# Kernel tuning notes

Measured on AMD Instinct MI355X. Metric: run time of the kernel, lower is better.

Reference implementation:

```python
import jax, jax.numpy as jnp
import numpy as np

M = 16
C = 7 * M          # 112, stage-8 channels
CLS = 20
TOPK = 3
NQ = 20000         # current-frame active sites at stage 8
NS = 8192          # support-frame active sites at stage 8
SCALE = 128.0      # voxel coordinate range at this depth


def setup_inputs() -> dict:
    key = jax.random.key(0)
    ks = jax.random.split(key, 9)
    coords_q = jax.random.uniform(ks[0], (NQ, 3), jnp.float32) * SCALE
    coords_s = jax.random.uniform(ks[1], (NS, 3), jnp.float32) * SCALE
    x7 = jax.random.normal(ks[2], (NQ, C), jnp.float32)
    feat_s7 = jax.random.normal(ks[3], (NS, C), jnp.float32)
    feat_s = jax.random.normal(ks[4], (NS, C), jnp.float32)
    w_attn = jax.random.normal(ks[5], (C,), jnp.float32) * 0.1
    W1 = jax.random.normal(ks[6], (2 * C, C), jnp.float32) * (1.0 / np.sqrt(2 * C))
    gamma = jnp.ones((C,), jnp.float32)
    beta = jnp.zeros((C,), jnp.float32)
    W2 = jax.random.normal(ks[7], (C, C), jnp.float32) * (1.0 / np.sqrt(C))
    W_cls = jax.random.normal(ks[8], (C, CLS), jnp.float32) * (1.0 / np.sqrt(C))
    b_cls = jnp.zeros((CLS,), jnp.float32)
    return dict(coords_q=coords_q, coords_s=coords_s, x7=x7, feat_s7=feat_s7,
                feat_s=feat_s, w_attn=w_attn, W1=W1, gamma=gamma, beta=beta,
                W2=W2, W_cls=W_cls, b_cls=b_cls)


def reference(coords_q, coords_s, x7, feat_s7, feat_s, w_attn, W1, gamma, beta, W2, W_cls, b_cls):
    # GlobalMeanAttentionPooling: attention-weighted mean over support sites -> global vector [C]
    a = jax.nn.softmax(feat_s7 @ w_attn)          # [NS]
    g = a @ feat_s7                                # [C]
    # GlobalMaskLayer: channel-wise sigmoid gating of current-frame features
    feat_q = x7 * jax.nn.sigmoid(g)                # [NQ, C]
    # DistMatchLayer_v4: top-3 nearest support voxels per query, softmax(-d2) weighting
    q2 = jnp.sum(coords_q * coords_q, -1, keepdims=True)   # [NQ, 1]
    s2 = jnp.sum(coords_s * coords_s, -1)                  # [NS]
    d2 = q2 + s2[None, :] - 2.0 * (coords_q @ coords_s.T)  # [NQ, NS]
    negd, idx = jax.lax.top_k(-d2, TOPK)                   # [NQ, K]
    w = jax.nn.softmax(negd, axis=-1)                      # [NQ, K]
    matched = jnp.einsum('nk,nkc->nc', w, feat_s[idx])     # [NQ, C]
    # tune_sub: 1x1 subconv (14m->7m) -> BN(eval affine) + ReLU -> 1x1 subconv (7m->7m)
    h = jnp.concatenate([feat_q, matched], -1) @ W1        # [NQ, C]
    h = jax.nn.relu(h * gamma + beta) @ W2                 # [NQ, C]
    # final classifier linear
    return h @ W_cls + b_cls                               # [NQ, CLS]
```

## Files before the change

kernel.cpp:

```cpp
#include <hip/hip_runtime.h>

#define NQv 20000
#define NSv 8192
#define Cv  112
#define CLSv 20
#define INFF 3.4e38f
#define JINF 0x7fffffff

#define GC 16
#define NCELL 4096
#define CELLH 8.0f
#define INVH 0.125f

#define POOLB 32
#define PT 1024
#define PNW (POOLB * PT / 64)

#define MB (NQv / 32)
#define MT 512
#define WS_START 3616
#define WS_PTS4  5668
#define WS_W1TH  38440
#define WS_W1TL  50984
#define WS_W2TH  63528
#define WS_W2TL  70696
#define WS_WCT   77864

typedef __attribute__((ext_vector_type(8))) short bf16x8;
typedef __attribute__((ext_vector_type(4))) float f32x4;
typedef unsigned short us;
typedef unsigned long long u64;

__device__ __forceinline__ float bf2f(us u) {
    union { unsigned int i; float f; } v; v.i = ((unsigned int)u) << 16; return v.f;
}
__device__ __forceinline__ us f2bf(float f) {
    union { float f; unsigned int i; } v; v.f = f;
    unsigned int r = v.i + 0x7fffu + ((v.i >> 16) & 1u);
    return (us)(r >> 16);
}
__device__ __forceinline__ void split(float v, us& h, us& l) {
    h = f2bf(v); l = f2bf(v - bf2f(h));
}

__device__ __forceinline__ u64 mkkey(float e, int j) {
    union { float f; unsigned int i; } v; v.f = e;
    unsigned int ue = v.i ^ ((unsigned int)((int)v.i >> 31) | 0x80000000u);
    return ((u64)ue << 32) | (unsigned int)j;
}
__device__ __forceinline__ float keyval(u64 k) {
    unsigned int ue = (unsigned int)(k >> 32);
    unsigned int u = ue ^ ((unsigned int)((int)(~ue) >> 31) | 0x80000000u);
    union { unsigned int i; float f; } v; v.i = u; return v.f;
}
__device__ __forceinline__ u64 umin64(u64 a, u64 b) { return a < b ? a : b; }
__device__ __forceinline__ u64 umax64(u64 a, u64 b) { return a > b ? a : b; }

__global__ __launch_bounds__(PT) void k_prep(const float* __restrict__ cs,
                                             const float* __restrict__ fs7,
                                             const float* __restrict__ wat,
                                             const float* __restrict__ W1,
                                             const float* __restrict__ W2,
                                             const float* __restrict__ Wc,
                                             float* __restrict__ ws) {
    int b = blockIdx.x, tid = threadIdx.x;

    if (b == POOLB + 1) {
        us* w1h = (us*)(ws + WS_W1TH);
        us* w1l = (us*)(ws + WS_W1TL);
        for (int idx = tid; idx < Cv * 224; idx += PT) {
            int c = idx / 224, k = idx - c * 224;
            us h, l; split(W1[k * Cv + c], h, l);
            w1h[c * 224 + k] = h; w1l[c * 224 + k] = l;
        }
        return;
    }
    if (b == POOLB + 2) {
        us* w2h = (us*)(ws + WS_W2TH);
        us* w2l = (us*)(ws + WS_W2TL);
        for (int idx = tid; idx < Cv * 128; idx += PT) {
            int c = idx >> 7, k = idx & 127;
            float v = (k < Cv) ? W2[k * Cv + c] : 0.f;
            us h, l; split(v, h, l);
            w2h[c * 128 + k] = h; w2l[c * 128 + k] = l;
        }
        float* wct = ws + WS_WCT;
        for (int idx = tid; idx < CLSv * Cv; idx += PT) {
            int cls = idx / Cv, k = idx - cls * Cv;
            wct[cls * Cv + k] = Wc[k * CLSv + cls];
        }
        return;
    }
    if (b == POOLB) {
        __shared__ int cnt[NCELL];
        __shared__ int wsum[PT / 64];
        us* startg = (us*)(ws + WS_START);
        float4* pts4 = (float4*)(ws + WS_PTS4);
        int lane = tid & 63, wv = tid >> 6;
        for (int i = tid; i < NCELL; i += PT) cnt[i] = 0;
        __syncthreads();
        float xx[8], yy[8], zz[8]; int cid[8]; int pp[8];
        #pragma unroll
        for (int k = 0; k < NSv / PT; ++k) {
            int p = k * PT + tid;
            pp[k] = p;
            xx[k] = cs[3 * p]; yy[k] = cs[3 * p + 1]; zz[k] = cs[3 * p + 2];
            int cx = (int)(xx[k] * INVH), cy = (int)(yy[k] * INVH), cz = (int)(zz[k] * INVH);
            cx = cx > 15 ? 15 : cx; cy = cy > 15 ? 15 : cy; cz = cz > 15 ? 15 : cz;
            cid[k] = (cz * GC + cy) * GC + cx;
            atomicAdd(&cnt[cid[k]], 1);
        }
        __syncthreads();
        int base = tid * 4;
        int c0 = cnt[base], c1 = cnt[base + 1], c2 = cnt[base + 2], c3 = cnt[base + 3];
        int local = c0 + c1 + c2 + c3;
        int inc = local;
        #pragma unroll
        for (int off = 1; off < 64; off <<= 1) {
            int v = __shfl_up(inc, off, 64);
            if (lane >= off) inc += v;
        }
        if (lane == 63) wsum[wv] = inc;
        __syncthreads();
        if (tid < PT / 64) {
            int v = wsum[tid];
            #pragma unroll
            for (int off = 1; off < 16; off <<= 1) {
                int o = __shfl_up(v, off, 64);
                if (tid >= off) v += o;
            }
            wsum[tid] = v;
        }
        __syncthreads();
        int wbase = (wv == 0) ? 0 : wsum[wv - 1];
        int run = wbase + inc - local;
        startg[base] = (us)run;     cnt[base] = run;     run += c0;
        startg[base + 1] = (us)run; cnt[base + 1] = run; run += c1;
        startg[base + 2] = (us)run; cnt[base + 2] = run; run += c2;
        startg[base + 3] = (us)run; cnt[base + 3] = run;
        if (tid == 0) startg[NCELL] = (us)NSv;
        __syncthreads();
        #pragma unroll
        for (int k = 0; k < NSv / PT; ++k) {
            int slot = atomicAdd(&cnt[cid[k]], 1);
            pts4[slot] = make_float4(-2.f * xx[k], -2.f * yy[k], -2.f * zz[k], (float)pp[k]);
        }
        return;
    }

    __shared__ float red[PT / 64][Cv + 1];
    int gtid = b * PT + tid;
    int wid = gtid >> 6, lw = tid >> 6, lane = gtid & 63, l2 = lane * 2;
    float2 wa = make_float2(0.f, 0.f);
    if (lane < 56) wa = *(const float2*)(wat + l2);
    float gx = 0.f, gy = 0.f, z = 0.f;
    for (int g = 0; g < 2; ++g) {
        float2 f[8]; float part[8];
        #pragma unroll
        for (int u = 0; u < 8; ++u) {
            int i = wid + (g * 8 + u) * PNW;
            f[u] = (lane < 56) ? *(const float2*)(fs7 + i * Cv + l2) : make_float2(0.f, 0.f);
            part[u] = f[u].x * wa.x + f[u].y * wa.y;
        }
        #pragma unroll
        for (int off = 32; off; off >>= 1)
            #pragma unroll
            for (int u = 0; u < 8; ++u) part[u] += __shfl_xor(part[u], off, 64);
        #pragma unroll
        for (int u = 0; u < 8; ++u) {
            float p = __expf(part[u]);
            gx = fmaf(p, f[u].x, gx); gy = fmaf(p, f[u].y, gy); z += p;
        }
    }
    if (lane < 56) { red[lw][l2] = gx; red[lw][l2 + 1] = gy; }
    if (lane == 0) red[lw][Cv] = z;
    __syncthreads();
    if (tid < Cv + 1) {
        float s = 0.f;
        #pragma unroll
        for (int i = 0; i < PT / 64; ++i) s += red[i][tid];
        ws[b * (Cv + 1) + tid] = s;
    }
}

__device__ __forceinline__ void scan_run(const float4* __restrict__ pts4,
                                         int a, int b, float qx, float qy, float qz,
                                         float& E0, float& E1, float& E2,
                                         int& J0, int& J1, int& J2) {
    for (int k = a; k < b; ++k) {
        float4 P = pts4[k];
        float x = -0.5f * P.x, y = -0.5f * P.y, z = -0.5f * P.z;
        float s2 = fmaf(x, x, fmaf(y, y, z * z));
        float e = fmaf(qx, P.x, fmaf(qy, P.y, fmaf(qz, P.z, s2)));
        int j = (int)P.w;
        bool lt2 = (e < E2) || (e == E2 && j < J2);
        if (lt2) {
            bool lt1 = (e < E1) || (e == E1 && j < J1);
            bool lt0 = (e < E0) || (e == E0 && j < J0);
            E2 = lt1 ? E1 : e;              J2 = lt1 ? J1 : j;
            E1 = lt0 ? E0 : (lt1 ? e : E1); J1 = lt0 ? J0 : (lt1 ? j : J1);
            if (lt0) { E0 = e; J0 = j; }
        }
    }
}

__global__ __launch_bounds__(MT, 6) void k_fused(
        const float* __restrict__ cq,
        const float* __restrict__ x7, const float* __restrict__ fs,
        const float* __restrict__ gma, const float* __restrict__ bta,
        const float* __restrict__ bc, const float* __restrict__ ws,
        float* __restrict__ out) {
    __shared__ __align__(16) us vb[2 * 32 * 232];
    __shared__ __align__(16) us hbh[32 * 136];
    __shared__ __align__(16) us hbl[32 * 136];
    __shared__ float gate[Cv];
    __shared__ int   qi[32][3];
    __shared__ float qw[32][3];

    us* vbh = vb;
    us* vbl = vb + 32 * 232;
    float* h2f = (float*)vb;

    const us* __restrict__ startg = (const us*)(ws + WS_START);
    const float4* __restrict__ pts4 = (const float4*)(ws + WS_PTS4);

    int tid = threadIdx.x;
    int q0 = blockIdx.x * 32;

    int vq = tid / 14, ve = tid - vq * 14;
    float4 px[4];
    bool hasx = (tid < 448) && (ve < 7);
    if (hasx) {
        const float4* xr = (const float4*)(x7 + (q0 + vq) * Cv + ve * 16);
        px[0] = xr[0]; px[1] = xr[1]; px[2] = xr[2]; px[3] = xr[3];
    }

    if (tid < Cv) {
        float st = 0.f, zt = 0.f;
        for (int b = 0; b < POOLB; ++b) {
            st += ws[b * (Cv + 1) + tid];
            zt += ws[b * (Cv + 1) + Cv];
        }
        gate[tid] = 1.0f / (1.0f + __expf(-(st / zt)));
    }
    {
        int q = tid >> 4, kk = Cv + (tid & 15);
        hbh[q * 136 + kk] = 0; hbl[q * 136 + kk] = 0;
    }

    {
        int sub = tid & 15;
        int qq  = tid >> 4;
        int q   = q0 + qq;
        float qx = cq[3 * q], qy = cq[3 * q + 1], qz = cq[3 * q + 2];
        float q2 = fmaf(qx, qx, fmaf(qy, qy, qz * qz));
        int cx = (int)(qx * INVH), cy = (int)(qy * INVH), cz = (int)(qz * INVH);
        cx = cx > 15 ? 15 : cx; cy = cy > 15 ? 15 : cy; cz = cz > 15 ? 15 : cz;
        float E0 = INFF, E1 = INFF, E2 = INFF;
        int   J0 = JINF, J1 = JINF, J2 = JINF;

        #pragma unroll
        for (int c = sub; c < 27; c += 16) {
            int dz = c / 9 - 1, dy = (c / 3) % 3 - 1, dx = c % 3 - 1;
            int xc = cx + dx, yc = cy + dy, zc = cz + dz;
            if ((unsigned)xc < 16u && (unsigned)yc < 16u && (unsigned)zc < 16u) {
                int ccell = (zc * GC + yc) * GC + xc;
                scan_run(pts4, startg[ccell], startg[ccell + 1], qx, qy, qz,
                         E0, E1, E2, J0, J1, J2);
            }
        }

        u64 K0 = ~0ull, K1 = ~0ull, K2 = ~0ull;
        bool done = false;
        for (int s = 2; ; ++s) {
            if (!done) {
                K0 = mkkey(E0, J0); K1 = mkkey(E1, J1); K2 = mkkey(E2, J2);
                #pragma unroll
                for (int off = 1; off < 16; off <<= 1) {
                    u64 b0 = __shfl_xor(K0, off, 64);
                    u64 b1 = __shfl_xor(K1, off, 64);
                    u64 b2 = __shfl_xor(K2, off, 64);
                    u64 xx = umax64(K0, b0), yy = umin64(K1, b1);
                    u64 zz = umax64(K1, b1), uu = umin64(K2, b2);
                    K0 = umin64(K0, b0);
                    u64 n1 = umin64(xx, yy);
                    K2 = umin64(umin64(umax64(xx, yy), zz), uu);
                    K1 = n1;
                }
            }
            if (s > 15) break;
            if (!done) {
                int r = s - 1;
                int xl = cx - r > 0 ? cx - r : 0, xh = cx + r < 15 ? cx + r : 15;
                int yl = cy - r > 0 ? cy - r : 0, yh = cy + r < 15 ? cy + r : 15;
                int zl = cz - r > 0 ? cz - r : 0, zh = cz + r < 15 ? cz + r : 15;
                float fx = INFF, fy = INFF, fz = INFF;
                if (xl > 0)  fx = qx - xl * CELLH;
                if (xh < 15) fx = fminf(fx, (xh + 1) * CELLH - qx);
                if (yl > 0)  fy = qy - yl * CELLH;
                if (yh < 15) fy = fminf(fy, (yh + 1) * CELLH - qy);
                if (zl > 0)  fz = qz - zl * CELLH;
                if (zh < 15) fz = fminf(fz, (zh + 1) * CELLH - qz);
                float dmin = fminf(fx, fminf(fy, fz));
                float t2 = keyval(K2);
                if (dmin * dmin > t2 + q2 + 0.5f) {
                    done = true;
                } else {
                    int side = 2 * s + 1, s2n = side * side, tot = s2n * side;
                    for (int idx = sub; idx < tot; idx += 16) {
                        int dz = idx / s2n - s;
                        int rem = idx - (dz + s) * s2n;
                        int dy = rem / side - s;
                        int dx = rem - (dy + s) * side - s;
                        int ax = dx < 0 ? -dx : dx, ay = dy < 0 ? -dy : dy, az = dz < 0 ? -dz : dz;
                        if (ax != s && ay != s && az != s) continue;
                        int xc = cx + dx, yc = cy + dy, zc = cz + dz;
                        if ((unsigned)xc > 15u || (unsigned)yc > 15u || (unsigned)zc > 15u) continue;
                        int ccell = (zc * GC + yc) * GC + xc;
                        scan_run(pts4, startg[ccell], startg[ccell + 1], qx, qy, qz,
                                 E0, E1, E2, J0, J1, J2);
                    }
                }
            }
            if (__all(done)) break;
        }

        if (sub == 0) {
            unsigned int A0 = (unsigned int)K0;
            unsigned int A1 = (unsigned int)K1;
            unsigned int A2 = (unsigned int)K2;
            if (A0 >= NSv) A0 = 0;
            if (A1 >= NSv) A1 = 0;
            if (A2 >= NSv) A2 = 0;
            float e0 = keyval(K0), e1 = keyval(K1), e2 = keyval(K2);
            float w1v = __expf(e0 - e1);
            float w2v = __expf(e0 - e2);
            float iw  = 1.0f / (1.0f + w1v + w2v);
            qw[qq][0] = iw; qw[qq][1] = w1v * iw; qw[qq][2] = w2v * iw;
            qi[qq][0] = (int)A0; qi[qq][1] = (int)A1; qi[qq][2] = (int)A2;
        }
    }
    __syncthreads();

    if (tid < 448) {
        int k0 = ve * 16;
        float vals[16];
        if (ve < 7) {
            #pragma unroll
            for (int i = 0; i < 4; ++i) {
                float4 v = px[i];
                vals[i * 4]     = v.x * gate[k0 + i * 4];
                vals[i * 4 + 1] = v.y * gate[k0 + i * 4 + 1];
                vals[i * 4 + 2] = v.z * gate[k0 + i * 4 + 2];
                vals[i * 4 + 3] = v.w * gate[k0 + i * 4 + 3];
            }
        } else {
            int kk = k0 - Cv;
            float w0 = qw[vq][0], w1v = qw[vq][1], w2v = qw[vq][2];
            const float4* r0 = (const float4*)(fs + qi[vq][0] * Cv + kk);
            const float4* r1 = (const float4*)(fs + qi[vq][1] * Cv + kk);
            const float4* r2 = (const float4*)(fs + qi[vq][2] * Cv + kk);
            #pragma unroll
            for (int i = 0; i < 4; ++i) {
                float4 a = r0[i], b = r1[i], c = r2[i];
                vals[i * 4]     = w0 * a.x + w1v * b.x + w2v * c.x;
                vals[i * 4 + 1] = w0 * a.y + w1v * b.y + w2v * c.y;
                vals[i * 4 + 2] = w0 * a.z + w1v * b.z + w2v * c.z;
                vals[i * 4 + 3] = w0 * a.w + w1v * b.w + w2v * c.w;
            }
        }
        #pragma unroll
        for (int i = 0; i < 16; ++i) {
            us h, l; split(vals[i], h, l);
            vbh[vq * 232 + k0 + i] = h;
            vbl[vq * 232 + k0 + i] = l;
        }
    }
    __syncthreads();

    int w = tid >> 6, lane = tid & 63, quad = lane >> 4, l16 = lane & 15;
    int cc = w * 16 + l16;

    if (w < 7) {
        f32x4 acc0 = {0.f, 0.f, 0.f, 0.f};
        f32x4 acc1 = {0.f, 0.f, 0.f, 0.f};
        const us* w1h = (const us*)(ws + WS_W1TH) + cc * 224;
        const us* w1l = (const us*)(ws + WS_W1TL) + cc * 224;
        #pragma unroll
        for (int ks = 0; ks < 7; ++ks) {
            int ko = ks * 32 + quad * 8;
            bf16x8 bh  = *(const bf16x8*)(w1h + ko);
            bf16x8 bl  = *(const bf16x8*)(w1l + ko);
            bf16x8 a0h = *(const bf16x8*)(vbh + l16 * 232 + ko);
            bf16x8 a0l = *(const bf16x8*)(vbl + l16 * 232 + ko);
            bf16x8 a1h = *(const bf16x8*)(vbh + (l16 + 16) * 232 + ko);
            bf16x8 a1l = *(const bf16x8*)(vbl + (l16 + 16) * 232 + ko);
            acc0 = __builtin_amdgcn_mfma_f32_16x16x32_bf16(a0h, bh, acc0, 0, 0, 0);
            acc0 = __builtin_amdgcn_mfma_f32_16x16x32_bf16(a0l, bh, acc0, 0, 0, 0);
            acc0 = __builtin_amdgcn_mfma_f32_16x16x32_bf16(a0h, bl, acc0, 0, 0, 0);
            acc1 = __builtin_amdgcn_mfma_f32_16x16x32_bf16(a1h, bh, acc1, 0, 0, 0);
            acc1 = __builtin_amdgcn_mfma_f32_16x16x32_bf16(a1l, bh, acc1, 0, 0, 0);
            acc1 = __builtin_amdgcn_mfma_f32_16x16x32_bf16(a1h, bl, acc1, 0, 0, 0);
        }
        float g = gma[cc], bb = bta[cc];
        #pragma unroll
        for (int r = 0; r < 4; ++r) {
            int q = quad * 4 + r;
            float h = fmaf(acc0[r], g, bb); h = h > 0.f ? h : 0.f;
            us hh, ll; split(h, hh, ll);
            hbh[q * 136 + cc] = hh; hbl[q * 136 + cc] = ll;
            float h2 = fmaf(acc1[r], g, bb); h2 = h2 > 0.f ? h2 : 0.f;
            split(h2, hh, ll);
            hbh[(q + 16) * 136 + cc] = hh; hbl[(q + 16) * 136 + cc] = ll;
        }
    }
    __syncthreads();

    if (w < 7) {
        f32x4 acc0 = {0.f, 0.f, 0.f, 0.f};
        f32x4 acc1 = {0.f, 0.f, 0.f, 0.f};
        const us* w2h = (const us*)(ws + WS_W2TH) + cc * 128;
        const us* w2l = (const us*)(ws + WS_W2TL) + cc * 128;
        #pragma unroll
        for (int ks = 0; ks < 4; ++ks) {
            int ko = ks * 32 + quad * 8;
            bf16x8 bh  = *(const bf16x8*)(w2h + ko);
            bf16x8 bl  = *(const bf16x8*)(w2l + ko);
            bf16x8 a0h = *(const bf16x8*)(hbh + l16 * 136 + ko);
            bf16x8 a0l = *(const bf16x8*)(hbl + l16 * 136 + ko);
            bf16x8 a1h = *(const bf16x8*)(hbh + (l16 + 16) * 136 + ko);
            bf16x8 a1l = *(const bf16x8*)(hbl + (l16 + 16) * 136 + ko);
            acc0 = __builtin_amdgcn_mfma_f32_16x16x32_bf16(a0h, bh, acc0, 0, 0, 0);
            acc0 = __builtin_amdgcn_mfma_f32_16x16x32_bf16(a0l, bh, acc0, 0, 0, 0);
            acc0 = __builtin_amdgcn_mfma_f32_16x16x32_bf16(a0h, bl, acc0, 0, 0, 0);
            acc1 = __builtin_amdgcn_mfma_f32_16x16x32_bf16(a1h, bh, acc1, 0, 0, 0);
            acc1 = __builtin_amdgcn_mfma_f32_16x16x32_bf16(a1l, bh, acc1, 0, 0, 0);
            acc1 = __builtin_amdgcn_mfma_f32_16x16x32_bf16(a1h, bl, acc1, 0, 0, 0);
        }
        #pragma unroll
        for (int r = 0; r < 4; ++r) {
            int q = quad * 4 + r;
            h2f[q * 116 + cc] = acc0[r];
            h2f[(q + 16) * 116 + cc] = acc1[r];
        }
    }
    __syncthreads();

    for (int it = tid; it < 32 * CLSv; it += MT) {
        int cls = it % CLSv, qq = it / CLSv;
        const float4* wr = (const float4*)(ws + WS_WCT + cls * Cv);
        const float4* hr = (const float4*)(h2f + qq * 116);
        float a = bc[cls];
        #pragma unroll 7
        for (int i = 0; i < 28; ++i) {
            float4 h = hr[i], v = wr[i];
            a = fmaf(h.x, v.x, fmaf(h.y, v.y, fmaf(h.z, v.z, fmaf(h.w, v.w, a))));
        }
        out[(q0 + qq) * CLSv + cls] = a;
    }
}

extern "C" void kernel_launch(void* const* d_in, const int* in_sizes, int n_in,
                              void* d_out, int out_size, void* d_ws, size_t ws_size,
                              hipStream_t stream) {
    const float* cq  = (const float*)d_in[0];
    const float* cs  = (const float*)d_in[1];
    const float* x7  = (const float*)d_in[2];
    const float* fs7 = (const float*)d_in[3];
    const float* fs  = (const float*)d_in[4];
    const float* wat = (const float*)d_in[5];
    const float* W1  = (const float*)d_in[6];
    const float* gma = (const float*)d_in[7];
    const float* bta = (const float*)d_in[8];
    const float* W2  = (const float*)d_in[9];
    const float* Wc  = (const float*)d_in[10];
    const float* bc  = (const float*)d_in[11];
    float* ws  = (float*)d_ws;
    float* out = (float*)d_out;

    k_prep<<<POOLB + 3, PT, 0, stream>>>(cs, fs7, wat, W1, W2, Wc, ws);
    k_fused<<<MB, MT, 0, stream>>>(cq, x7, fs, gma, bta, bc, ws, out);
}
```

Measured before the change: 142.5 us.

## Halve queries per block to 16 and remap MFMA waves to column pairs

The fused kernel now handles 16 queries per block with 256 threads, which doubles the block count. In the two MFMA GEMMs each of the 4 waves now covers one 16-row tile and one or two 16-column output tiles, instead of 7 waves each covering two row tiles. The pooling partials are stored channel-major so the gate reduction reads contiguous memory, and the s==2 shell of the kNN search gets a specialized loop with constant divisors. The intent is better load balance and occupancy for the irregular kNN search, at the cost of reloading weight fragments per 16 queries and some wave imbalance (waves 0-2 do double work).

```diff
diff --git a/kernel.cpp b/kernel.cpp
--- a/kernel.cpp
+++ b/kernel.cpp
@@ -16,8 +16,9 @@
 #define PT 1024
 #define PNW (POOLB * PT / 64)
 
-#define MB (NQv / 32)
-#define MT 512
+#define MQ 16
+#define MB (NQv / MQ)
+#define MT 256
 #define WS_START 3616
 #define WS_PTS4  5668
 #define WS_W1TH  38440
@@ -179,7 +180,7 @@
         float s = 0.f;
         #pragma unroll
         for (int i = 0; i < PT / 64; ++i) s += red[i][tid];
-        ws[b * (Cv + 1) + tid] = s;
+        ws[tid * POOLB + b] = s;
     }
 }
 
@@ -210,26 +211,26 @@
         const float* __restrict__ gma, const float* __restrict__ bta,
         const float* __restrict__ bc, const float* __restrict__ ws,
         float* __restrict__ out) {
-    __shared__ __align__(16) us vb[2 * 32 * 232];
-    __shared__ __align__(16) us hbh[32 * 136];
-    __shared__ __align__(16) us hbl[32 * 136];
+    __shared__ __align__(16) us vb[2 * MQ * 232];
+    __shared__ __align__(16) us hbh[MQ * 136];
+    __shared__ __align__(16) us hbl[MQ * 136];
     __shared__ float gate[Cv];
-    __shared__ int   qi[32][3];
-    __shared__ float qw[32][3];
+    __shared__ int   qi[MQ][3];
+    __shared__ float qw[MQ][3];
 
     us* vbh = vb;
-    us* vbl = vb + 32 * 232;
+    us* vbl = vb + MQ * 232;
     float* h2f = (float*)vb;
 
     const us* __restrict__ startg = (const us*)(ws + WS_START);
     const float4* __restrict__ pts4 = (const float4*)(ws + WS_PTS4);
 
     int tid = threadIdx.x;
-    int q0 = blockIdx.x * 32;
+    int q0 = blockIdx.x * MQ;
 
     int vq = tid / 14, ve = tid - vq * 14;
     float4 px[4];
-    bool hasx = (tid < 448) && (ve < 7);
+    bool hasx = (tid < 224) && (ve < 7);
     if (hasx) {
         const float4* xr = (const float4*)(x7 + (q0 + vq) * Cv + ve * 16);
         px[0] = xr[0]; px[1] = xr[1]; px[2] = xr[2]; px[3] = xr[3];
@@ -237,10 +238,10 @@
 
     if (tid < Cv) {
         float st = 0.f, zt = 0.f;
-        for (int b = 0; b < POOLB; ++b) {
-            st += ws[b * (Cv + 1) + tid];
-            zt += ws[b * (Cv + 1) + Cv];
-        }
+        const float* pr = ws + tid * POOLB;
+        const float* zr = ws + Cv * POOLB;
+        #pragma unroll
+        for (int b = 0; b < POOLB; ++b) { st += pr[b]; zt += zr[b]; }
         gate[tid] = 1.0f / (1.0f + __expf(-(st / zt)));
     }
     {
@@ -305,6 +306,20 @@
                 float t2 = keyval(K2);
                 if (dmin * dmin > t2 + q2 + 0.5f) {
                     done = true;
+                } else if (s == 2) {
+                    for (int idx = sub; idx < 125; idx += 16) {
+                        int dz = idx / 25 - 2;
+                        int rem = idx - (dz + 2) * 25;
+                        int dy = rem / 5 - 2;
+                        int dx = rem - (dy + 2) * 5 - 2;
+                        int ax = dx < 0 ? -dx : dx, ay = dy < 0 ? -dy : dy, az = dz < 0 ? -dz : dz;
+                        if (ax != 2 && ay != 2 && az != 2) continue;
+                        int xc = cx + dx, yc = cy + dy, zc = cz + dz;
+                        if ((unsigned)xc > 15u || (unsigned)yc > 15u || (unsigned)zc > 15u) continue;
+                        int ccell = (zc * GC + yc) * GC + xc;
+                        scan_run(pts4, startg[ccell], startg[ccell + 1], qx, qy, qz,
+                                 E0, E1, E2, J0, J1, J2);
+                    }
                 } else {
                     int side = 2 * s + 1, s2n = side * side, tot = s2n * side;
                     for (int idx = sub; idx < tot; idx += 16) {
@@ -342,7 +357,7 @@
     }
     __syncthreads();
 
-    if (tid < 448) {
+    if (tid < 224) {
         int k0 = ve * 16;
         float vals[16];
         if (ve < 7) {
@@ -379,74 +394,87 @@
     __syncthreads();
 
     int w = tid >> 6, lane = tid & 63, quad = lane >> 4, l16 = lane & 15;
-    int cc = w * 16 + l16;
-
-    if (w < 7) {
+    bool two = (w < 3);
+    int cc0 = w * 16 + l16;
+    int cc1 = two ? (w + 4) * 16 + l16 : cc0;
+
+    {
         f32x4 acc0 = {0.f, 0.f, 0.f, 0.f};
         f32x4 acc1 = {0.f, 0.f, 0.f, 0.f};
-        const us* w1h = (const us*)(ws + WS_W1TH) + cc * 224;
-        const us* w1l = (const us*)(ws + WS_W1TL) + cc * 224;
+        const us* w1h0 = (const us*)(ws + WS_W1TH) + cc0 * 224;
+        const us* w1l0 = (const us*)(ws + WS_W1TL) + cc0 * 224;
+        const us* w1h1 = (const us*)(ws + WS_W1TH) + cc1 * 224;
+        const us* w1l1 = (const us*)(ws + WS_W1TL) + cc1 * 224;
         #pragma unroll
         for (int ks = 0; ks < 7; ++ks) {
             int ko = ks * 32 + quad * 8;
-            bf16x8 bh  = *(const bf16x8*)(w1h + ko);
-            bf16x8 bl  = *(const bf16x8*)(w1l + ko);
-            bf16x8 a0h = *(const bf16x8*)(vbh + l16 * 232 + ko);
-            bf16x8 a0l = *(const bf16x8*)(vbl + l16 * 232 + ko);
-            bf16x8 a1h = *(const bf16x8*)(vbh + (l16 + 16) * 232 + ko);
-            bf16x8 a1l = *(const bf16x8*)(vbl + (l16 + 16) * 232 + ko);
-            acc0 = __builtin_amdgcn_mfma_f32_16x16x32_bf16(a0h, bh, acc0, 0, 0, 0);
-            acc0 = __builtin_amdgcn_mfma_f32_16x16x32_bf16(a0l, bh, acc0, 0, 0, 0);
-            acc0 = __builtin_amdgcn_mfma_f32_16x16x32_bf16(a0h, bl, acc0, 0, 0, 0);
-            acc1 = __builtin_amdgcn_mfma_f32_16x16x32_bf16(a1h, bh, acc1, 0, 0, 0);
-            acc1 = __builtin_amdgcn_mfma_f32_16x16x32_bf16(a1l, bh, acc1, 0, 0, 0);
-            acc1 = __builtin_amdgcn_mfma_f32_16x16x32_bf16(a1h, bl, acc1, 0, 0, 0);
-        }
-        float g = gma[cc], bb = bta[cc];
+            bf16x8 ah = *(const bf16x8*)(vbh + l16 * 232 + ko);
+            bf16x8 al = *(const bf16x8*)(vbl + l16 * 232 + ko);
+            bf16x8 bh0 = *(const bf16x8*)(w1h0 + ko);
+            bf16x8 bl0 = *(const bf16x8*)(w1l0 + ko);
+            acc0 = __builtin_amdgcn_mfma_f32_16x16x32_bf16(ah, bh0, acc0, 0, 0, 0);
+            acc0 = __builtin_amdgcn_mfma_f32_16x16x32_bf16(al, bh0, acc0, 0, 0, 0);
+            acc0 = __builtin_amdgcn_mfma_f32_16x16x32_bf16(ah, bl0, acc0, 0, 0, 0);
+            if (two) {
+                bf16x8 bh1 = *(const bf16x8*)(w1h1 + ko);
+                bf16x8 bl1 = *(const bf16x8*)(w1l1 + ko);
+                acc1 = __builtin_amdgcn_mfma_f32_16x16x32_bf16(ah, bh1, acc1, 0, 0, 0);
+                acc1 = __builtin_amdgcn_mfma_f32_16x16x32_bf16(al, bh1, acc1, 0, 0, 0);
+                acc1 = __builtin_amdgcn_mfma_f32_16x16x32_bf16(ah, bl1, acc1, 0, 0, 0);
+            }
+        }
+        float g0 = gma[cc0], b0 = bta[cc0];
+        float g1 = two ? gma[cc1] : 0.f, b1 = two ? bta[cc1] : 0.f;
         #pragma unroll
         for (int r = 0; r < 4; ++r) {
             int q = quad * 4 + r;
-            float h = fmaf(acc0[r], g, bb); h = h > 0.f ? h : 0.f;
+            float h = fmaf(acc0[r], g0, b0); h = h > 0.f ? h : 0.f;
             us hh, ll; split(h, hh, ll);
-            hbh[q * 136 + cc] = hh; hbl[q * 136 + cc] = ll;
-            float h2 = fmaf(acc1[r], g, bb); h2 = h2 > 0.f ? h2 : 0.f;
-            split(h2, hh, ll);
-            hbh[(q + 16) * 136 + cc] = hh; hbl[(q + 16) * 136 + cc] = ll;
+            hbh[q * 136 + cc0] = hh; hbl[q * 136 + cc0] = ll;
+            if (two) {
+                float h2 = fmaf(acc1[r], g1, b1); h2 = h2 > 0.f ? h2 : 0.f;
+                split(h2, hh, ll);
+                hbh[q * 136 + cc1] = hh; hbl[q * 136 + cc1] = ll;
+            }
         }
     }
     __syncthreads();
 
-    if (w < 7) {
+    {
         f32x4 acc0 = {0.f, 0.f, 0.f, 0.f};
         f32x4 acc1 = {0.f, 0.f, 0.f, 0.f};
-        const us* w2h = (const us*)(ws + WS_W2TH) + cc * 128;
-        const us* w2l = (const us*)(ws + WS_W2TL) + cc * 128;
+        const us* w2h0 = (const us*)(ws + WS_W2TH) + cc0 * 128;
+        const us* w2l0 = (const us*)(ws + WS_W2TL) + cc0 * 128;
+        const us* w2h1 = (const us*)(ws + WS_W2TH) + cc1 * 128;
+        const us* w2l1 = (const us*)(ws + WS_W2TL) + cc1 * 128;
         #pragma unroll
         for (int ks = 0; ks < 4; ++ks) {
             int ko = ks * 32 + quad * 8;
-            bf16x8 bh  = *(const bf16x8*)(w2h + ko);
-            bf16x8 bl  = *(const bf16x8*)(w2l + ko);
-            bf16x8 a0h = *(const bf16x8*)(hbh + l16 * 136 + ko);
-            bf16x8 a0l = *(const bf16x8*)(hbl + l16 * 136 + ko);
-            bf16x8 a1h = *(const bf16x8*)(hbh + (l16 + 16) * 136 + ko);
-            bf16x8 a1l = *(const bf16x8*)(hbl + (l16 + 16) * 136 + ko);
-            acc0 = __builtin_amdgcn_mfma_f32_16x16x32_bf16(a0h, bh, acc0, 0, 0, 0);
-            acc0 = __builtin_amdgcn_mfma_f32_16x16x32_bf16(a0l, bh, acc0, 0, 0, 0);
-            acc0 = __builtin_amdgcn_mfma_f32_16x16x32_bf16(a0h, bl, acc0, 0, 0, 0);
-            acc1 = __builtin_amdgcn_mfma_f32_16x16x32_bf16(a1h, bh, acc1, 0, 0, 0);
-            acc1 = __builtin_amdgcn_mfma_f32_16x16x32_bf16(a1l, bh, acc1, 0, 0, 0);
-            acc1 = __builtin_amdgcn_mfma_f32_16x16x32_bf16(a1h, bl, acc1, 0, 0, 0);
+            bf16x8 ah = *(const bf16x8*)(hbh + l16 * 136 + ko);
+            bf16x8 al = *(const bf16x8*)(hbl + l16 * 136 + ko);
+            bf16x8 bh0 = *(const bf16x8*)(w2h0 + ko);
+            bf16x8 bl0 = *(const bf16x8*)(w2l0 + ko);
+            acc0 = __builtin_amdgcn_mfma_f32_16x16x32_bf16(ah, bh0, acc0, 0, 0, 0);
+            acc0 = __builtin_amdgcn_mfma_f32_16x16x32_bf16(al, bh0, acc0, 0, 0, 0);
+            acc0 = __builtin_amdgcn_mfma_f32_16x16x32_bf16(ah, bl0, acc0, 0, 0, 0);
+            if (two) {
+                bf16x8 bh1 = *(const bf16x8*)(w2h1 + ko);
+                bf16x8 bl1 = *(const bf16x8*)(w2l1 + ko);
+                acc1 = __builtin_amdgcn_mfma_f32_16x16x32_bf16(ah, bh1, acc1, 0, 0, 0);
+                acc1 = __builtin_amdgcn_mfma_f32_16x16x32_bf16(al, bh1, acc1, 0, 0, 0);
+                acc1 = __builtin_amdgcn_mfma_f32_16x16x32_bf16(ah, bl1, acc1, 0, 0, 0);
+            }
         }
         #pragma unroll
         for (int r = 0; r < 4; ++r) {
             int q = quad * 4 + r;
-            h2f[q * 116 + cc] = acc0[r];
-            h2f[(q + 16) * 116 + cc] = acc1[r];
+            h2f[q * 116 + cc0] = acc0[r];
+            if (two) h2f[q * 116 + cc1] = acc1[r];
         }
     }
     __syncthreads();
 
-    for (int it = tid; it < 32 * CLSv; it += MT) {
+    for (int it = tid; it < MQ * CLSv; it += MT) {
         int cls = it % CLSv, qq = it / CLSv;
         const float4* wr = (const float4*)(ws + WS_WCT + cls * Cv);
         const float4* hr = (const float4*)(h2f + qq * 116);
```

After: 144.0 us. Within noise of the previous version (+1.0%).
